# Kernel tuning notes

Hardware: AMD Instinct MI355X
Metric: run time of the kernel (lower is better)

The kernel has to match this reference:

```python
import jax, jax.numpy as jnp
import numpy as np

D = 32            # dims[0] == dims[1] (modes per register)
K = 8             # kernel_size (filter interferometer modes)
STRIDE = 8        # stride (== kernel_size -> block-diagonal register)
N_BLOCKS = (D - K) // STRIDE + 1          # filters per register = 4
N_PHI = K * (K - 1) // 2                  # Reck triangle: one Ry BS per crossing = 28
BATCH = 16


def _filter_unitary(phi):
    """K-mode Reck-triangle interferometer of BS.Ry(theta=-2*phi) gates.
    Each gate mixes adjacent modes (j-1, j) with the real rotation
    [[cos phi, sin phi], [-sin phi, cos phi]]. Returns real [K, K] orthogonal."""
    U = jnp.eye(K, dtype=phi.dtype)
    idx = 0
    for i in range(1, K):
        for j in range(i, 0, -1):
            c, s = jnp.cos(phi[idx]), jnp.sin(phi[idx])
            r0 = c * U[j - 1] + s * U[j]
            r1 = -s * U[j - 1] + c * U[j]
            U = U.at[j - 1].set(r0).at[j].set(r1)
            idx += 1
    return U


def _register_unitary(phi):
    """D-mode register: the SAME filter unitary (shared params) placed every
    STRIDE modes; identity on any leftover modes. Block-diagonal [D, D]."""
    uf = _filter_unitary(phi)
    U = jnp.eye(D, dtype=phi.dtype)
    for b in range(N_BLOCKS):
        o = b * STRIDE
        U = U.at[o:o + K, o:o + K].set(uf)
    return U


def setup_inputs() -> dict:
    key = jax.random.key(0)
    k1, k2, k3 = jax.random.split(key, 3)
    two_pi = jnp.float32(2.0 * np.pi)
    return {
        "rho": jax.random.normal(k1, (BATCH, D * D, D * D), dtype=jnp.float32),
        "phi_x": two_pi * jax.random.uniform(k2, (N_PHI,), dtype=jnp.float32),
        "phi_y": two_pi * jax.random.uniform(k3, (N_PHI,), dtype=jnp.float32),
    }


def reference(rho, phi_x, phi_y):
    # u = kron(u_x, u_y) : [D^2, D^2] real orthogonal (BS circuit => real)
    u = jnp.kron(_register_unitary(phi_x), _register_unitary(phi_y))
    # new_rho = u @ rho @ u^dagger ; real => dagger is transpose
    u_rho = jnp.einsum('ij,bjk->bik', u, rho)   # [b, D^2, D^2]
    return u_rho @ u.T
```

## Files before the change

kernel.cpp:

```cpp
#include <hip/hip_runtime.h>
#include <math.h>


__global__ void setup_uf(const float* __restrict__ phi_x,
                         const float* __restrict__ phi_y,
                         float* __restrict__ ws) {
    const int t = threadIdx.x;
    if (t < 2) {
        const float* phi = (t == 0) ? phi_x : phi_y;
        float U[8][8];
#pragma unroll
        for (int i = 0; i < 8; ++i)
#pragma unroll
            for (int j = 0; j < 8; ++j) U[i][j] = (i == j) ? 1.0f : 0.0f;
        int idx = 0;
#pragma unroll
        for (int i = 1; i < 8; ++i) {
#pragma unroll
            for (int j = i; j >= 1; --j) {
                const float c = cosf(phi[idx]);
                const float s = sinf(phi[idx]);
#pragma unroll
                for (int m = 0; m < 8; ++m) {
                    const float a = U[j - 1][m], b = U[j][m];
                    U[j - 1][m] = c * a + s * b;
                    U[j][m]     = -s * a + c * b;
                }
                ++idx;
            }
        }
        float* o = ws + t * 64;
#pragma unroll
        for (int i = 0; i < 8; ++i)
#pragma unroll
            for (int j = 0; j < 8; ++j) o[i * 8 + j] = U[i][j];
    }
}

#define CONTRACT_INNER(M, a)                                                   \
    _Pragma("unroll")                                                          \
    for (int _g = 0; _g < 8; ++_g) {                                           \
        float _tmp[8];                                                         \
        _Pragma("unroll")                                                      \
        for (int _i = 0; _i < 8; ++_i) {                                       \
            float _acc = 0.0f;                                                 \
            _Pragma("unroll")                                                  \
            for (int _k = 0; _k < 8; ++_k)                                     \
                _acc = fmaf((M)[_i * 8 + _k], (a)[_g * 8 + _k], _acc);         \
            _tmp[_i] = _acc;                                                   \
        }                                                                      \
        _Pragma("unroll")                                                      \
        for (int _i = 0; _i < 8; ++_i) (a)[_g * 8 + _i] = _tmp[_i];            \
    }

#define CONTRACT_OUTER(M, a)                                                   \
    _Pragma("unroll")                                                          \
    for (int _g = 0; _g < 8; ++_g) {                                           \
        float _tmp[8];                                                         \
        _Pragma("unroll")                                                      \
        for (int _i = 0; _i < 8; ++_i) {                                       \
            float _acc = 0.0f;                                                 \
            _Pragma("unroll")                                                  \
            for (int _k = 0; _k < 8; ++_k)                                     \
                _acc = fmaf((M)[_i * 8 + _k], (a)[_k * 8 + _g], _acc);         \
            _tmp[_i] = _acc;                                                   \
        }                                                                      \
        _Pragma("unroll")                                                      \
        for (int _i = 0; _i < 8; ++_i) (a)[_i * 8 + _g] = _tmp[_i];            \
    }

__device__ __forceinline__ void col_phase(const float* __restrict__ S,
                                          const float* __restrict__ UX,
                                          const float* __restrict__ UY,
                                          float* __restrict__ out,
                                          size_t B0, int rowbase, int bx2,
                                          int rr, int by2) {
    const int r2 = rr & 31;
    const int r7 = r2 & 7;
    float p[64];
#pragma unroll
    for (int x = 0; x < 8; ++x) {
        const int cc0 = (((x * 8 + by2 * 2 + 0) ^ r7) << 2);
        const int cc1 = (((x * 8 + by2 * 2 + 1) ^ r7) << 2);
        const float4 q0 = *reinterpret_cast<const float4*>(&S[r2 * 256 + cc0]);
        const float4 q1 = *reinterpret_cast<const float4*>(&S[r2 * 256 + cc1]);
        p[x * 8 + 0] = q0.x; p[x * 8 + 1] = q0.y;
        p[x * 8 + 2] = q0.z; p[x * 8 + 3] = q0.w;
        p[x * 8 + 4] = q1.x; p[x * 8 + 5] = q1.y;
        p[x * 8 + 6] = q1.z; p[x * 8 + 7] = q1.w;
    }

    CONTRACT_INNER(UY, p)
    CONTRACT_OUTER(UX, p)

    const int gr = rowbase + ((rr >> 3) * 32) + (rr & 7);
    float* __restrict__ dst = out + B0 + (size_t)gr * 1024 + bx2 * 256 + by2 * 8;
#pragma unroll
    for (int x = 0; x < 8; ++x) {
        *reinterpret_cast<float4*>(dst + x * 32) =
            make_float4(p[x * 8 + 0], p[x * 8 + 1], p[x * 8 + 2], p[x * 8 + 3]);
        *reinterpret_cast<float4*>(dst + x * 32 + 4) =
            make_float4(p[x * 8 + 4], p[x * 8 + 5], p[x * 8 + 6], p[x * 8 + 7]);
    }
}

__global__ __launch_bounds__(256, 4) void qconv_fused(const float* __restrict__ rho,
                                                      const float* __restrict__ ws,
                                                      float* __restrict__ out) {
    __shared__ float S[8192];
    const int t   = threadIdx.x;
    const int bid = blockIdx.x;
    const int bx2 = bid & 3;
    const int by1 = (bid >> 2) & 3;
    const int bx1 = (bid >> 4) & 3;
    const int b   = bid >> 6;

    const float* __restrict__ UX = ws;
    const float* __restrict__ UY = ws + 64;

    const size_t B0      = (size_t)b << 20;
    const int    rowbase = bx1 * 256 + by1 * 8;
    const int    cg      = bx2 * 256 + t;

    const float* __restrict__ src = rho + B0 + (size_t)rowbase * 1024 + cg;
    float v[64];
#pragma unroll
    for (int i = 0; i < 8; ++i)
#pragma unroll
        for (int j = 0; j < 8; ++j)
            v[i * 8 + j] = src[(i * 32 + j) * 1024];

    CONTRACT_INNER(UY, v)
    CONTRACT_OUTER(UX, v)

    int cswz[8];
#pragma unroll
    for (int r7 = 0; r7 < 8; ++r7)
        cswz[r7] = ((((t >> 2) ^ r7) << 2) | (t & 3));

#pragma unroll
    for (int r = 0; r < 32; ++r) S[r * 256 + cswz[r & 7]] = v[r];
    __syncthreads();

    const int wid = t >> 6;
    if (wid < 2) {
        col_phase(S, UX, UY, out, B0, rowbase, bx2, t & 31, t >> 5);
    }
    __syncthreads();

#pragma unroll
    for (int r = 32; r < 64; ++r) S[(r - 32) * 256 + cswz[r & 7]] = v[r];
    __syncthreads();

    if (wid >= 2) {
        const int u = t - 128;
        col_phase(S, UX, UY, out, B0, rowbase, bx2, 32 + (u & 31), u >> 5);
    }
}

extern "C" void kernel_launch(void* const* d_in, const int* in_sizes, int n_in,
                              void* d_out, int out_size, void* d_ws, size_t ws_size,
                              hipStream_t stream) {
    const float* rho   = (const float*)d_in[0];
    const float* phi_x = (const float*)d_in[1];
    const float* phi_y = (const float*)d_in[2];
    float* out = (float*)d_out;
    float* ws  = (float*)d_ws;

    setup_uf<<<1, 64, 0, stream>>>(phi_x, phi_y, ws);
    qconv_fused<<<1024, 256, 0, stream>>>(rho, ws, out);
}
```

Measured before the change: 43.81 us.

## Split column-phase work across all 256 threads in both LDS halves

Previously only half of the block's threads ran the column-phase contraction in each LDS half, leaving the other 128 threads idle. Now every thread does half of the output rows for the outer (UX) index in both phases: it reads a full 8x8 patch, applies UY, and accumulates into 4 of the 8 output rows. This doubles the active lanes in the second stage at the cost of reading each LDS row twice and repeating the UY contraction in both thread halves. The launch-bounds occupancy hint of 4 is also dropped, which may change register allocation and occupancy.

After: 49.07 us. 1.12x slower.

```diff
diff --git a/kernel.cpp b/kernel.cpp
--- a/kernel.cpp
+++ b/kernel.cpp
@@ -69,44 +69,62 @@
         for (int _i = 0; _i < 8; ++_i) (a)[_i * 8 + _g] = _tmp[_i];            \
     }
 
-__device__ __forceinline__ void col_phase(const float* __restrict__ S,
-                                          const float* __restrict__ UX,
-                                          const float* __restrict__ UY,
-                                          float* __restrict__ out,
-                                          size_t B0, int rowbase, int bx2,
-                                          int rr, int by2) {
-    const int r2 = rr & 31;
-    const int r7 = r2 & 7;
-    float p[64];
+__device__ __forceinline__ void consume_half(const float* __restrict__ S,
+                                             const float* __restrict__ UX,
+                                             const float* __restrict__ UY,
+                                             float* __restrict__ out,
+                                             size_t B0, int rowbase, int bx2,
+                                             int t, int base) {
+    const int rr5   = t & 31;
+    const int by2   = (t >> 5) & 3;
+    const int ihalf = t >> 7;
+    const int r7    = rr5 & 7;
+    const float* __restrict__ Srow = S + rr5 * 256;
+
+    float q[32];
 #pragma unroll
-    for (int x = 0; x < 8; ++x) {
-        const int cc0 = (((x * 8 + by2 * 2 + 0) ^ r7) << 2);
-        const int cc1 = (((x * 8 + by2 * 2 + 1) ^ r7) << 2);
-        const float4 q0 = *reinterpret_cast<const float4*>(&S[r2 * 256 + cc0]);
-        const float4 q1 = *reinterpret_cast<const float4*>(&S[r2 * 256 + cc1]);
-        p[x * 8 + 0] = q0.x; p[x * 8 + 1] = q0.y;
-        p[x * 8 + 2] = q0.z; p[x * 8 + 3] = q0.w;
-        p[x * 8 + 4] = q1.x; p[x * 8 + 5] = q1.y;
-        p[x * 8 + 6] = q1.z; p[x * 8 + 7] = q1.w;
+    for (int k = 0; k < 8; ++k) {
+        const int c0 = (((k * 8 + by2 * 2 + 0) ^ r7) << 2);
+        const int c1 = (((k * 8 + by2 * 2 + 1) ^ r7) << 2);
+        const float4 a = *reinterpret_cast<const float4*>(&Srow[c0]);
+        const float4 bq = *reinterpret_cast<const float4*>(&Srow[c1]);
+        float raw[8] = {a.x, a.y, a.z, a.w, bq.x, bq.y, bq.z, bq.w};
+        float w[8];
+#pragma unroll
+        for (int jj = 0; jj < 8; ++jj) {
+            float acc = 0.0f;
+#pragma unroll
+            for (int j = 0; j < 8; ++j)
+                acc = fmaf(UY[jj * 8 + j], raw[j], acc);
+            w[jj] = acc;
+        }
+#pragma unroll
+        for (int ii = 0; ii < 4; ++ii) {
+            const float ux = UX[(ihalf * 4 + ii) * 8 + k];
+#pragma unroll
+            for (int jj = 0; jj < 8; ++jj) {
+                if (k == 0) q[ii * 8 + jj] = ux * w[jj];
+                else        q[ii * 8 + jj] = fmaf(ux, w[jj], q[ii * 8 + jj]);
+            }
+        }
     }
 
-    CONTRACT_INNER(UY, p)
-    CONTRACT_OUTER(UX, p)
-
+    const int rr = base + rr5;
     const int gr = rowbase + ((rr >> 3) * 32) + (rr & 7);
-    float* __restrict__ dst = out + B0 + (size_t)gr * 1024 + bx2 * 256 + by2 * 8;
+    float* __restrict__ dst =
+        out + B0 + (size_t)gr * 1024 + bx2 * 256 + by2 * 8 + ihalf * 128;
 #pragma unroll
-    for (int x = 0; x < 8; ++x) {
-        *reinterpret_cast<float4*>(dst + x * 32) =
-            make_float4(p[x * 8 + 0], p[x * 8 + 1], p[x * 8 + 2], p[x * 8 + 3]);
-        *reinterpret_cast<float4*>(dst + x * 32 + 4) =
-            make_float4(p[x * 8 + 4], p[x * 8 + 5], p[x * 8 + 6], p[x * 8 + 7]);
+    for (int ii = 0; ii < 4; ++ii) {
+        *reinterpret_cast<float4*>(dst + ii * 32) =
+            make_float4(q[ii * 8 + 0], q[ii * 8 + 1], q[ii * 8 + 2], q[ii * 8 + 3]);
+        *reinterpret_cast<float4*>(dst + ii * 32 + 4) =
+            make_float4(q[ii * 8 + 4], q[ii * 8 + 5], q[ii * 8 + 6], q[ii * 8 + 7]);
     }
 }
 
-__global__ __launch_bounds__(256, 4) void qconv_fused(const float* __restrict__ rho,
-                                                      const float* __restrict__ ws,
-                                                      float* __restrict__ out) {
+__global__ __launch_bounds__(256) void qconv_fused(const float* __restrict__ rho,
+                                                   const float* __restrict__ ws,
+                                                   float* __restrict__ out) {
     __shared__ float S[8192];
     const int t   = threadIdx.x;
     const int bid = blockIdx.x;
@@ -123,12 +141,13 @@
     const int    cg      = bx2 * 256 + t;
 
     const float* __restrict__ src = rho + B0 + (size_t)rowbase * 1024 + cg;
+
     float v[64];
 #pragma unroll
     for (int i = 0; i < 8; ++i)
 #pragma unroll
         for (int j = 0; j < 8; ++j)
-            v[i * 8 + j] = src[(i * 32 + j) * 1024];
+            v[i * 8 + j] = src[(size_t)(i * 32 + j) * 1024];
 
     CONTRACT_INNER(UY, v)
     CONTRACT_OUTER(UX, v)
@@ -141,21 +160,13 @@
 #pragma unroll
     for (int r = 0; r < 32; ++r) S[r * 256 + cswz[r & 7]] = v[r];
     __syncthreads();
-
-    const int wid = t >> 6;
-    if (wid < 2) {
-        col_phase(S, UX, UY, out, B0, rowbase, bx2, t & 31, t >> 5);
-    }
+    consume_half(S, UX, UY, out, B0, rowbase, bx2, t, 0);
     __syncthreads();
 
 #pragma unroll
     for (int r = 32; r < 64; ++r) S[(r - 32) * 256 + cswz[r & 7]] = v[r];
     __syncthreads();
-
-    if (wid >= 2) {
-        const int u = t - 128;
-        col_phase(S, UX, UY, out, B0, rowbase, bx2, 32 + (u & 31), u >> 5);
-    }
+    consume_half(S, UX, UY, out, B0, rowbase, bx2, t, 32);
 }
 
 extern "C" void kernel_launch(void* const* d_in, const int* in_sizes, int n_in,
```
